# Performance work log

Hardware: AMD Instinct MI355X
Metric: run time of the kernel (lower is better)

## Reference

```python
import jax, jax.numpy as jnp
import numpy as np

D_MODEL = 768
D_INNER = 1536
D_STATE = 16
D_CONV = 4
DT_RANK = 48
N_LAYER = 4
VOCAB = 32000
B, L = 2, 1024


def rmsnorm(x, w, eps=1e-5):
    return x * jax.lax.rsqrt(jnp.mean(x * x, axis=-1, keepdims=True) + eps) * w


def depthwise_causal_conv(u, w):
    # u: (b, l, d_in), w: (d_in, k). torch pads both sides then truncates to l,
    # which equals left-pad by k-1 (causal).
    b, l, d = u.shape
    k = w.shape[1]
    up = jnp.pad(u, ((0, 0), (k - 1, 0), (0, 0)))
    out = jnp.zeros_like(u)
    for i in range(k):
        out = out + up[:, i:i + l, :] * w[:, i]
    return out


def selective_scan(u, delta, A, Bm, C, Dp):
    # u,delta: (b,l,d_in); A: (d_in,n); Bm,C: (b,l,n); Dp: (d_in,)
    dA = jnp.exp(delta[..., None] * A)                      # (b,l,d,n)
    dBu = delta[..., None] * Bm[:, :, None, :] * u[..., None]

    def step(h, inp):
        dA_t, dBu_t, C_t = inp
        h = dA_t * h + dBu_t                                 # (b,d,n)
        y = jnp.einsum('bdn,bn->bd', h, C_t)
        return h, y

    h0 = jnp.zeros_like(dA[:, 0])
    xs = (jnp.moveaxis(dA, 1, 0), jnp.moveaxis(dBu, 1, 0), jnp.moveaxis(C, 1, 0))
    _, ys = jax.lax.scan(step, h0, xs)                       # (l,b,d)
    return jnp.moveaxis(ys, 0, 1) + u * Dp


def setup_inputs() -> dict:
    key = jax.random.key(0)
    ks = jax.random.split(key, 16)
    s = lambda fan: 1.0 / np.sqrt(fan)
    inp = {}
    inp['text_input'] = jax.random.randint(ks[0], (B, L), 0, VOCAB)
    inp['visual_input'] = jax.random.normal(ks[1], (B, L, D_MODEL), dtype=jnp.float32)
    inp['embedding'] = jax.random.normal(ks[2], (VOCAB, D_MODEL), dtype=jnp.float32) * 0.02
    inp['norm_w'] = jnp.ones((N_LAYER, D_MODEL), dtype=jnp.float32)
    inp['norm_f_w'] = jnp.ones((D_MODEL,), dtype=jnp.float32)
    inp['in_proj_w'] = jax.random.normal(ks[3], (N_LAYER, 2 * D_INNER, D_MODEL)) * s(D_MODEL)
    inp['in_proj2_w'] = jax.random.normal(ks[4], (N_LAYER, D_INNER, D_MODEL)) * s(D_MODEL)
    inp['conv_w'] = jax.random.normal(ks[5], (N_LAYER, D_INNER, D_CONV)) * s(D_CONV)
    inp['conv_b'] = jax.random.normal(ks[6], (N_LAYER, D_INNER)) * 0.01
    inp['x_proj_w'] = jax.random.normal(ks[7], (N_LAYER, DT_RANK + D_STATE, D_INNER)) * s(D_INNER)
    inp['c_proj_w'] = jax.random.normal(ks[8], (N_LAYER, D_STATE, D_INNER)) * s(D_INNER)
    inp['dt_proj_w'] = jax.random.normal(ks[9], (N_LAYER, D_INNER, DT_RANK)) * s(DT_RANK)
    inp['dt_proj_b'] = jax.random.normal(ks[10], (N_LAYER, D_INNER)) * 0.01
    A = jnp.tile(jnp.arange(1, D_STATE + 1, dtype=jnp.float32)[None, :], (D_INNER, 1))
    inp['A_log'] = jnp.tile(jnp.log(A)[None], (N_LAYER, 1, 1))
    inp['D'] = jnp.ones((N_LAYER, D_INNER), dtype=jnp.float32)
    inp['out_proj_w'] = jax.random.normal(ks[11], (N_LAYER, D_MODEL, D_INNER)) * s(D_INNER)
    return inp


def reference(text_input, visual_input, embedding, norm_w, norm_f_w, in_proj_w,
              in_proj2_w, conv_w, conv_b, x_proj_w, c_proj_w, dt_proj_w,
              dt_proj_b, A_log, D, out_proj_w):
    x = embedding[text_input]  # (b,l,d_model)
    n_layer = A_log.shape[0]
    l = x.shape[1]
    for i in range(n_layer):
        q = rmsnorm(x, norm_w[i])
        v = rmsnorm(visual_input, norm_w[i])
        xr = q @ in_proj_w[i].T                               # (b,l,2*d_inner)
        vin = v @ in_proj2_w[i].T                             # (b,l,d_inner)
        t, res = jnp.split(xr, 2, axis=-1)
        t = depthwise_causal_conv(t, conv_w[i]) + conv_b[i]
        t = jax.nn.silu(t)
        # ssm
        A = -jnp.exp(A_log[i])
        x_dbl = t @ x_proj_w[i].T                             # (b,l,dt_rank+n)
        delta, Bm = jnp.split(x_dbl, [DT_RANK], axis=-1)
        C = vin @ c_proj_w[i].T                               # (b,l,n)
        delta = jax.nn.softplus(delta @ dt_proj_w[i].T + dt_proj_b[i])
        y = selective_scan(t, delta, A, Bm, C, D[i])
        y = y * jax.nn.silu(res)
        x = y @ out_proj_w[i].T + x
    x = rmsnorm(x, norm_f_w)
    return x @ embedding.T  # tied lm_head -> (b,l,vocab)
```

## Files before the change

kernel.cpp:

```cpp
#include <hip/hip_runtime.h>
#include <hip/hip_bf16.h>
#include <math.h>

#define B_ 2
#define L_ 1024
#define DM 768
#define DI 1536
#define DS 16
#define DR 48
#define NL 4
#define VOC 32000
#define BL (B_*L_)
#define NCH 32
#define LCH (L_/NCH)
#define KSPLIT 4

typedef __attribute__((ext_vector_type(8))) short short8;
typedef __attribute__((ext_vector_type(4))) float f32x4;

__device__ __forceinline__ float sigmoidf_(float x){ return 1.f/(1.f+expf(-x)); }
__device__ __forceinline__ float siluf_(float x){ return x*sigmoidf_(x); }
__device__ __forceinline__ float softplusf_(float x){ return fmaxf(x,0.f) + log1pf(expf(-fabsf(x))); }
__device__ __forceinline__ unsigned short f2bf(float f){
    unsigned u = __float_as_uint(f);
    u += 0x7FFFu + ((u >> 16) & 1u);
    return (unsigned short)(u >> 16);
}
__device__ __forceinline__ float bf2f(unsigned short h){
    return __uint_as_float((unsigned)h << 16);
}
__device__ __forceinline__ void gload_lds16(const unsigned short* g, unsigned short* l){
    __builtin_amdgcn_global_load_lds(
        (const __attribute__((address_space(1))) void*)g,
        (__attribute__((address_space(3))) void*)l, 16, 0, 0);
}

__global__ void cast_bf16_kernel(const float* __restrict__ in, unsigned short* __restrict__ out, int n4)
{
    for (int i = blockIdx.x*256 + threadIdx.x; i < n4; i += gridDim.x*256) {
        float4 v = ((const float4*)in)[i];
        ushort4 o;
        o.x = f2bf(v.x); o.y = f2bf(v.y); o.z = f2bf(v.z); o.w = f2bf(v.w);
        ((ushort4*)out)[i] = o;
    }
}

__global__ void cast_pair_kernel(const float* __restrict__ in,
                                 unsigned short* __restrict__ hi,
                                 unsigned short* __restrict__ lo, int n4)
{
    for (int i = blockIdx.x*256 + threadIdx.x; i < n4; i += gridDim.x*256) {
        float4 v = ((const float4*)in)[i];
        ushort4 h, l;
        h.x = f2bf(v.x); l.x = f2bf(v.x - bf2f(h.x));
        h.y = f2bf(v.y); l.y = f2bf(v.y - bf2f(h.y));
        h.z = f2bf(v.z); l.z = f2bf(v.z - bf2f(h.z));
        h.w = f2bf(v.w); l.w = f2bf(v.w - bf2f(h.w));
        ((ushort4*)hi)[i] = h;
        ((ushort4*)lo)[i] = l;
    }
}

__global__ void embed_kernel(const int* __restrict__ idx, const float* __restrict__ emb,
                             float* __restrict__ x)
{
    int i = blockIdx.x*256 + threadIdx.x;
    if (i >= BL*DM) return;
    int c = i % DM; int bl = i / DM;
    x[i] = emb[(size_t)idx[bl]*DM + c];
}

template<int MODE>
__global__ void rmsnorm_kernel(const float* __restrict__ in, const float* __restrict__ w,
                               void* __restrict__ outv, void* __restrict__ outv2)
{
    int row = blockIdx.x;
    const float* xr = in + (size_t)row*DM;
    float ss = 0.f;
    for (int c = threadIdx.x; c < DM; c += 256) { float v = xr[c]; ss += v*v; }
    #pragma unroll
    for (int o = 32; o > 0; o >>= 1) ss += __shfl_down(ss, o, 64);
    __shared__ float red[4];
    if ((threadIdx.x & 63) == 0) red[threadIdx.x >> 6] = ss;
    __syncthreads();
    float tot = red[0] + red[1] + red[2] + red[3];
    float scale = rsqrtf(tot * (1.f/DM) + 1e-5f);
    for (int c = threadIdx.x; c < DM; c += 256) {
        float v = xr[c]*scale*w[c];
        if (MODE == 0) ((float*)outv)[(size_t)row*DM + c] = v;
        else if (MODE == 1) ((unsigned short*)outv)[(size_t)row*DM + c] = f2bf(v);
        else {
            unsigned short h = f2bf(v);
            ((unsigned short*)outv)[(size_t)row*DM + c]  = h;
            ((unsigned short*)outv2)[(size_t)row*DM + c] = f2bf(v - bf2f(h));
        }
    }
}

template<int EPI>
__global__ __launch_bounds__(256) void gemm_mfma(
    const unsigned short* __restrict__ A, int lda,
    const unsigned short* __restrict__ W, int ldb,
    float* __restrict__ C, int ldc,
    const float* __restrict__ extra,
    int K)
{
    __shared__ unsigned short As[128*64];
    __shared__ unsigned short Bs[128*64];
    const int tid = threadIdx.x;
    const int bm = blockIdx.y*128, bn = blockIdx.x*128;
    const int l  = tid & 63;
    const int w  = tid >> 6;
    const int wr = (w >> 1)*64, wc = (w & 1)*64;
    const int lr = l & 15, lg = l >> 4;

    f32x4 zero4 = {0.f, 0.f, 0.f, 0.f};
    f32x4 acc[4][4];
    #pragma unroll
    for (int m = 0; m < 4; m++)
        #pragma unroll
        for (int n = 0; n < 4; n++) acc[m][n] = zero4;

    for (int k0 = 0; k0 < K; k0 += 64) {
        __syncthreads();
        #pragma unroll
        for (int i = 0; i < 4; i++) {
            int c   = i*256 + tid;
            int row = c >> 3;
            int kb  = c & 7;
            int kbs = (kb ^ (row & 7)) << 3;
            gload_lds16(A + (size_t)(bm+row)*lda + k0 + kbs, &As[c*8]);
            gload_lds16(W + (size_t)(bn+row)*ldb + k0 + kbs, &Bs[c*8]);
        }
        __syncthreads();
        #pragma unroll
        for (int kk = 0; kk < 2; kk++) {
            short8 af[4], bfr[4];
            #pragma unroll
            for (int m = 0; m < 4; m++) {
                int row = wr + m*16 + lr;
                int kb  = kk*4 + lg;
                af[m] = *(const short8*)&As[row*64 + ((kb ^ (row & 7)) << 3)];
            }
            #pragma unroll
            for (int n = 0; n < 4; n++) {
                int row = wc + n*16 + lr;
                int kb  = kk*4 + lg;
                bfr[n] = *(const short8*)&Bs[row*64 + ((kb ^ (row & 7)) << 3)];
            }
            #pragma unroll
            for (int m = 0; m < 4; m++)
                #pragma unroll
                for (int n = 0; n < 4; n++)
                    acc[m][n] = __builtin_amdgcn_mfma_f32_16x16x32_bf16(af[m], bfr[n], acc[m][n], 0, 0, 0);
        }
    }

    #pragma unroll
    for (int m = 0; m < 4; m++) {
        #pragma unroll
        for (int n = 0; n < 4; n++) {
            int col = bn + wc + n*16 + lr;
            #pragma unroll
            for (int r = 0; r < 4; r++) {
                int rowi = bm + wr + m*16 + lg*4 + r;
                float v = acc[m][n][r];
                if (EPI == 1) v += extra[(size_t)rowi*ldc + col];
                C[(size_t)rowi*ldc + col] = v;
            }
        }
    }
}

template<int EPI>
__global__ __launch_bounds__(256) void gemm_mfma2(
    const unsigned short* __restrict__ Ah, const unsigned short* __restrict__ Alo, int lda,
    const unsigned short* __restrict__ Wh, const unsigned short* __restrict__ Wlo, int ldb,
    float* __restrict__ C, int ldc,
    const float* __restrict__ extra,
    int K)
{
    __shared__ unsigned short Ash[128*64];
    __shared__ unsigned short Asl[128*64];
    __shared__ unsigned short Bsh[128*64];
    __shared__ unsigned short Bsl[128*64];
    const int tid = threadIdx.x;
    const int bm = blockIdx.y*128, bn = blockIdx.x*128;
    const int l  = tid & 63;
    const int w  = tid >> 6;
    const int wr = (w >> 1)*64, wc = (w & 1)*64;
    const int lr = l & 15, lg = l >> 4;

    f32x4 zero4 = {0.f, 0.f, 0.f, 0.f};
    f32x4 acc[4][4];
    #pragma unroll
    for (int m = 0; m < 4; m++)
        #pragma unroll
        for (int n = 0; n < 4; n++) acc[m][n] = zero4;

    for (int k0 = 0; k0 < K; k0 += 64) {
        __syncthreads();
        #pragma unroll
        for (int i = 0; i < 4; i++) {
            int c   = i*256 + tid;
            int row = c >> 3;
            int kb  = c & 7;
            int kbs = (kb ^ (row & 7)) << 3;
            const size_t ao = (size_t)(bm+row)*lda + k0 + kbs;
            const size_t bo = (size_t)(bn+row)*ldb + k0 + kbs;
            gload_lds16(Ah  + ao, &Ash[c*8]);
            gload_lds16(Alo + ao, &Asl[c*8]);
            gload_lds16(Wh  + bo, &Bsh[c*8]);
            gload_lds16(Wlo + bo, &Bsl[c*8]);
        }
        __syncthreads();
        #pragma unroll
        for (int kk = 0; kk < 2; kk++) {
            short8 ah[4], al[4], bh[4], bl[4];
            #pragma unroll
            for (int m = 0; m < 4; m++) {
                int row = wr + m*16 + lr;
                int so  = row*64 + (((kk*4 + lg) ^ (row & 7)) << 3);
                ah[m] = *(const short8*)&Ash[so];
                al[m] = *(const short8*)&Asl[so];
            }
            #pragma unroll
            for (int n = 0; n < 4; n++) {
                int row = wc + n*16 + lr;
                int so  = row*64 + (((kk*4 + lg) ^ (row & 7)) << 3);
                bh[n] = *(const short8*)&Bsh[so];
                bl[n] = *(const short8*)&Bsl[so];
            }
            #pragma unroll
            for (int m = 0; m < 4; m++)
                #pragma unroll
                for (int n = 0; n < 4; n++) {
                    acc[m][n] = __builtin_amdgcn_mfma_f32_16x16x32_bf16(al[m], bh[n], acc[m][n], 0, 0, 0);
                    acc[m][n] = __builtin_amdgcn_mfma_f32_16x16x32_bf16(ah[m], bl[n], acc[m][n], 0, 0, 0);
                    acc[m][n] = __builtin_amdgcn_mfma_f32_16x16x32_bf16(ah[m], bh[n], acc[m][n], 0, 0, 0);
                }
        }
    }

    #pragma unroll
    for (int m = 0; m < 4; m++) {
        #pragma unroll
        for (int n = 0; n < 4; n++) {
            int col = bn + wc + n*16 + lr;
            #pragma unroll
            for (int r = 0; r < 4; r++) {
                int rowi = bm + wr + m*16 + lg*4 + r;
                float v = acc[m][n][r];
                if (EPI == 1) v += extra[(size_t)rowi*ldc + col];
                C[(size_t)rowi*ldc + col] = v;
            }
        }
    }
}

template<int EPI>
__global__ __launch_bounds__(256) void gemm_tile(
    const float* __restrict__ A, int lda,
    const float* __restrict__ W, int ldb,
    float* __restrict__ C, int ldc,
    const float* __restrict__ extra,
    int K)
{
    __shared__ float As[8][128];
    __shared__ float Bs[8][128];
    const int bm = blockIdx.y * 128;
    const int bn = blockIdx.x * 128;
    const int tid = threadIdx.x;
    const int lr = tid >> 1;
    const int lh = (tid & 1) * 4;
    const int tr = tid >> 4;
    const int tc = tid & 15;

    float acc[8][8];
    #pragma unroll
    for (int i = 0; i < 8; i++)
        #pragma unroll
        for (int j = 0; j < 8; j++) acc[i][j] = 0.f;

    const float* Arow = A + (size_t)(bm + lr)*lda + lh;
    const float* Wrow = W + (size_t)(bn + lr)*ldb + lh;

    for (int k0 = 0; k0 < K; k0 += 8) {
        float4 av = *(const float4*)(Arow + k0);
        float4 wv = *(const float4*)(Wrow + k0);
        __syncthreads();
        As[lh+0][lr] = av.x; As[lh+1][lr] = av.y; As[lh+2][lr] = av.z; As[lh+3][lr] = av.w;
        Bs[lh+0][lr] = wv.x; Bs[lh+1][lr] = wv.y; Bs[lh+2][lr] = wv.z; Bs[lh+3][lr] = wv.w;
        __syncthreads();
        #pragma unroll
        for (int k = 0; k < 8; k++) {
            float a[8], b[8];
            *(float4*)(a)   = *(const float4*)&As[k][tr*8];
            *(float4*)(a+4) = *(const float4*)&As[k][tr*8+4];
            *(float4*)(b)   = *(const float4*)&Bs[k][tc*8];
            *(float4*)(b+4) = *(const float4*)&Bs[k][tc*8+4];
            #pragma unroll
            for (int i = 0; i < 8; i++)
                #pragma unroll
                for (int j = 0; j < 8; j++)
                    acc[i][j] = fmaf(a[i], b[j], acc[i][j]);
        }
    }

    #pragma unroll
    for (int i = 0; i < 8; i++) {
        int row = bm + tr*8 + i;
        float* crow = C + (size_t)row*ldc + bn + tc*8;
        float v[8];
        if (EPI == 2) {
            const float* bia = extra + bn + tc*8;
            #pragma unroll
            for (int j = 0; j < 8; j++) v[j] = softplusf_(acc[i][j] + bia[j]);
        } else {
            #pragma unroll
            for (int j = 0; j < 8; j++) v[j] = acc[i][j];
        }
        *(float4*)(crow)   = make_float4(v[0],v[1],v[2],v[3]);
        *(float4*)(crow+4) = make_float4(v[4],v[5],v[6],v[7]);
    }
}

__global__ __launch_bounds__(256) void gemm_skinny(
    const float* __restrict__ A, int lda,
    const float* __restrict__ W, int ldb,
    float* __restrict__ partial,
    int M, int N, int K)
{
    int klen = K / gridDim.z;
    int kbeg = blockIdx.z * klen;
    __shared__ float As[64][33];
    __shared__ float Ws[16][33];
    int tid = threadIdx.x;
    int bm = blockIdx.y*64, bn = blockIdx.x*16;
    int ar = tid >> 2, ak = (tid & 3)*8;
    int wr = tid >> 4, wk = (tid & 15)*2;
    int tr = tid >> 4, tc = tid & 15;

    float acc[4] = {0.f,0.f,0.f,0.f};
    for (int k0 = kbeg; k0 < kbeg + klen; k0 += 32) {
        float4 a0 = *(const float4*)(A + (size_t)(bm+ar)*lda + k0 + ak);
        float4 a1 = *(const float4*)(A + (size_t)(bm+ar)*lda + k0 + ak + 4);
        float2 wv = *(const float2*)(W + (size_t)(bn+wr)*ldb + k0 + wk);
        __syncthreads();
        As[ar][ak+0]=a0.x; As[ar][ak+1]=a0.y; As[ar][ak+2]=a0.z; As[ar][ak+3]=a0.w;
        As[ar][ak+4]=a1.x; As[ar][ak+5]=a1.y; As[ar][ak+6]=a1.z; As[ar][ak+7]=a1.w;
        Ws[wr][wk] = wv.x; Ws[wr][wk+1] = wv.y;
        __syncthreads();
        #pragma unroll 8
        for (int k = 0; k < 32; k++) {
            float b = Ws[tc][k];
            #pragma unroll
            for (int i = 0; i < 4; i++) acc[i] = fmaf(As[tr*4+i][k], b, acc[i]);
        }
    }
    #pragma unroll
    for (int i = 0; i < 4; i++)
        partial[((size_t)blockIdx.z*M + bm + tr*4 + i)*N + bn + tc] = acc[i];
}

__global__ void reduce_splitk(const float* __restrict__ partial, float* __restrict__ out, int MN)
{
    int i = blockIdx.x*256 + threadIdx.x;
    if (i >= MN) return;
    float s = 0.f;
    #pragma unroll
    for (int z = 0; z < KSPLIT; z++) s += partial[(size_t)z*MN + i];
    out[i] = s;
}

__global__ void conv_silu_kernel(const float* __restrict__ xr, const float* __restrict__ cw,
                                 const float* __restrict__ cb, float* __restrict__ t)
{
    int i = blockIdx.x*256 + threadIdx.x;
    if (i >= BL*DI) return;
    int d = i % DI; int bl = i / DI; int l = bl % L_; int b = bl / L_;
    const float* base = xr + (size_t)b*L_*(2*DI);
    float acc = cb[d];
    #pragma unroll
    for (int q = 0; q < 4; q++) {
        int ll = l - 3 + q;
        if (ll >= 0) acc = fmaf(base[(size_t)ll*(2*DI) + d], cw[d*4+q], acc);
    }
    t[i] = siluf_(acc);
}

__global__ void scan_p1(const float* __restrict__ delta, const float* __restrict__ t,
                        const float* __restrict__ xdbl, const float* __restrict__ A_log,
                        float* __restrict__ Aprod, float* __restrict__ Bacc)
{
    int idx = blockIdx.x*256 + threadIdx.x;
    if (idx >= B_*NCH*DI) return;
    int d = idx % DI; int c = (idx/DI) % NCH; int b = idx/(DI*NCH);
    float Ad[16];
    #pragma unroll
    for (int n = 0; n < 16; n++) Ad[n] = -expf(A_log[d*16+n]);
    float P[16], S[16];
    #pragma unroll
    for (int n = 0; n < 16; n++) { P[n] = 1.f; S[n] = 0.f; }
    for (int s = 0; s < LCH; s++) {
        int bl = b*L_ + c*LCH + s;
        float dt = delta[(size_t)bl*DI + d];
        float u  = t[(size_t)bl*DI + d];
        const float* Bp = xdbl + (size_t)bl*64 + 48;
        #pragma unroll
        for (int n = 0; n < 16; n++) {
            float a  = expf(dt*Ad[n]);
            float bu = dt*Bp[n]*u;
            P[n] *= a;
            S[n] = fmaf(a, S[n], bu);
        }
    }
    size_t o = (size_t)idx*16;
    #pragma unroll
    for (int n = 0; n < 16; n++) { Aprod[o+n] = P[n]; Bacc[o+n] = S[n]; }
}

__global__ void scan_p2(const float* __restrict__ Aprod, const float* __restrict__ Bacc,
                        float* __restrict__ Hinit)
{
    int idx = blockIdx.x*256 + threadIdx.x;
    if (idx >= B_*DI) return;
    int d = idx % DI, b = idx / DI;
    float h[16];
    #pragma unroll
    for (int n = 0; n < 16; n++) h[n] = 0.f;
    for (int c = 0; c < NCH; c++) {
        size_t o = (((size_t)b*NCH + c)*DI + d)*16;
        #pragma unroll
        for (int n = 0; n < 16; n++) Hinit[o+n] = h[n];
        #pragma unroll
        for (int n = 0; n < 16; n++) h[n] = fmaf(Aprod[o+n], h[n], Bacc[o+n]);
    }
}

__global__ void scan_p3(const float* __restrict__ delta, const float* __restrict__ t,
                        const float* __restrict__ xdbl, const float* __restrict__ Cb,
                        const float* __restrict__ A_log, const float* __restrict__ Dp,
                        const float* __restrict__ Hinit, const float* __restrict__ xr,
                        unsigned short* __restrict__ zh, unsigned short* __restrict__ zl)
{
    int idx = blockIdx.x*256 + threadIdx.x;
    if (idx >= B_*NCH*DI) return;
    int d = idx % DI; int c = (idx/DI) % NCH; int b = idx/(DI*NCH);
    float Ad[16];
    #pragma unroll
    for (int n = 0; n < 16; n++) Ad[n] = -expf(A_log[d*16+n]);
    float h[16];
    size_t ho = (size_t)idx*16;
    #pragma unroll
    for (int n = 0; n < 16; n++) h[n] = Hinit[ho+n];
    float Dd = Dp[d];
    for (int s = 0; s < LCH; s++) {
        int bl = b*L_ + c*LCH + s;
        float dt = delta[(size_t)bl*DI + d];
        float u  = t[(size_t)bl*DI + d];
        const float* Bp = xdbl + (size_t)bl*64 + 48;
        const float* Cp = Cb + (size_t)bl*16;
        float y = 0.f;
        #pragma unroll
        for (int n = 0; n < 16; n++) {
            float a = expf(dt*Ad[n]);
            h[n] = fmaf(a, h[n], dt*Bp[n]*u);
            y = fmaf(h[n], Cp[n], y);
        }
        y = fmaf(u, Dd, y);
        float r = xr[(size_t)bl*(2*DI) + DI + d];
        float zv = y * siluf_(r);
        unsigned short hh = f2bf(zv);
        zh[(size_t)bl*DI + d] = hh;
        zl[(size_t)bl*DI + d] = f2bf(zv - bf2f(hh));
    }
}

extern "C" void kernel_launch(void* const* d_in, const int* in_sizes, int n_in,
                              void* d_out, int out_size, void* d_ws, size_t ws_size,
                              hipStream_t stream)
{
    const int*   text     = (const int*)  d_in[0];
    const float* visual   = (const float*)d_in[1];
    const float* emb      = (const float*)d_in[2];
    const float* norm_w   = (const float*)d_in[3];
    const float* norm_f_w = (const float*)d_in[4];
    const float* in_proj  = (const float*)d_in[5];
    const float* in_proj2 = (const float*)d_in[6];
    const float* conv_w   = (const float*)d_in[7];
    const float* conv_b   = (const float*)d_in[8];
    const float* x_proj   = (const float*)d_in[9];
    const float* c_proj   = (const float*)d_in[10];
    const float* dt_w     = (const float*)d_in[11];
    const float* dt_b     = (const float*)d_in[12];
    const float* A_log    = (const float*)d_in[13];
    const float* Dp       = (const float*)d_in[14];
    const float* out_proj = (const float*)d_in[15];
    float* out = (float*)d_out;

    float* ws = (float*)d_ws;
    size_t off = 0;
    float* x     = ws + off; off += (size_t)BL*DM;
    float* xr    = ws + off; off += (size_t)BL*2*DI;
    float* vin   = ws + off; off += (size_t)BL*DI;
    float* tb    = ws + off; off += (size_t)BL*DI;
    float* dl    = ws + off; off += (size_t)BL*DI;
    float* xdbl  = ws + off; off += (size_t)BL*64;
    float* Cb    = ws + off; off += (size_t)BL*16;
    float* Aprod = ws + off; off += (size_t)B_*NCH*DI*DS;
    float* Bacc  = ws + off; off += (size_t)B_*NCH*DI*DS;
    float* Hinit = ws + off; off += (size_t)B_*NCH*DI*DS;
    float* part  = ws + off; off += (size_t)KSPLIT*BL*64;

    unsigned short* bfb = (unsigned short*)(ws + off);
    size_t bo = 0;
    unsigned short* emb_bf = bfb + bo; bo += (size_t)VOC*DM;
    unsigned short* wA_h   = bfb + bo; bo += (size_t)2*DI*DM;
    unsigned short* wA_l   = bfb + bo; bo += (size_t)2*DI*DM;
    unsigned short* wB_h   = bfb + bo; bo += (size_t)DI*DM;
    unsigned short* wB_l   = bfb + bo; bo += (size_t)DI*DM;
    unsigned short* wO_h   = bfb + bo; bo += (size_t)DM*DI;
    unsigned short* wO_l   = bfb + bo; bo += (size_t)DM*DI;
    unsigned short* q_h    = bfb + bo; bo += (size_t)BL*DM;
    unsigned short* q_l    = bfb + bo; bo += (size_t)BL*DM;
    unsigned short* v_h    = bfb + bo; bo += (size_t)BL*DM;
    unsigned short* v_l    = bfb + bo; bo += (size_t)BL*DM;
    unsigned short* z_h    = bfb + bo; bo += (size_t)BL*DI;
    unsigned short* z_l    = bfb + bo; bo += (size_t)BL*DI;
    unsigned short* xn_bf  = bfb + bo; bo += (size_t)BL*DM;

    dim3 blk(256);
    dim3 cgrid(2048);

    cast_bf16_kernel<<<cgrid, blk, 0, stream>>>(emb, emb_bf, VOC*DM/4);

    embed_kernel<<<dim3((BL*DM)/256), blk, 0, stream>>>(text, emb, x);

    for (int i = 0; i < NL; i++) {
        const float* nw = norm_w + (size_t)i*DM;
        rmsnorm_kernel<2><<<dim3(BL), blk, 0, stream>>>(x, nw, q_h, q_l);
        rmsnorm_kernel<2><<<dim3(BL), blk, 0, stream>>>(visual, nw, v_h, v_l);

        cast_pair_kernel<<<cgrid, blk, 0, stream>>>(in_proj  + (size_t)i*2*DI*DM, wA_h, wA_l, 2*DI*DM/4);
        cast_pair_kernel<<<cgrid, blk, 0, stream>>>(in_proj2 + (size_t)i*DI*DM,   wB_h, wB_l, DI*DM/4);
        cast_pair_kernel<<<cgrid, blk, 0, stream>>>(out_proj + (size_t)i*DM*DI,   wO_h, wO_l, DM*DI/4);

        gemm_mfma2<0><<<dim3(2*DI/128, BL/128), blk, 0, stream>>>(
            q_h, q_l, DM, wA_h, wA_l, DM, xr, 2*DI, nullptr, DM);
        gemm_mfma2<0><<<dim3(DI/128, BL/128), blk, 0, stream>>>(
            v_h, v_l, DM, wB_h, wB_l, DM, vin, DI, nullptr, DM);

        conv_silu_kernel<<<dim3((BL*DI)/256), blk, 0, stream>>>(
            xr, conv_w + (size_t)i*DI*4, conv_b + (size_t)i*DI, tb);

        gemm_skinny<<<dim3(64/16, BL/64, KSPLIT), blk, 0, stream>>>(
            tb, DI, x_proj + (size_t)i*(DR+DS)*DI, DI, part, BL, 64, DI);
        reduce_splitk<<<dim3((BL*64)/256), blk, 0, stream>>>(part, xdbl, BL*64);

        gemm_skinny<<<dim3(1, BL/64, KSPLIT), blk, 0, stream>>>(
            vin, DI, c_proj + (size_t)i*DS*DI, DI, part, BL, 16, DI);
        reduce_splitk<<<dim3((BL*16)/256), blk, 0, stream>>>(part, Cb, BL*16);

        gemm_tile<2><<<dim3(DI/128, BL/128), blk, 0, stream>>>(
            xdbl, 64, dt_w + (size_t)i*DI*DR, DR, dl, DI, dt_b + (size_t)i*DI, DR);

        const float* Al = A_log + (size_t)i*DI*DS;
        scan_p1<<<dim3((B_*NCH*DI)/256), blk, 0, stream>>>(dl, tb, xdbl, Al, Aprod, Bacc);
        scan_p2<<<dim3((B_*DI+255)/256), blk, 0, stream>>>(Aprod, Bacc, Hinit);
        scan_p3<<<dim3((B_*NCH*DI)/256), blk, 0, stream>>>(dl, tb, xdbl, Cb, Al,
            Dp + (size_t)i*DI, Hinit, xr, z_h, z_l);

        gemm_mfma2<1><<<dim3(DM/128, BL/128), blk, 0, stream>>>(
            z_h, z_l, DI, wO_h, wO_l, DI, x, DM, x, DI);
    }

    rmsnorm_kernel<1><<<dim3(BL), blk, 0, stream>>>(x, norm_f_w, xn_bf, nullptr);
    gemm_mfma<0><<<dim3(VOC/128, BL/128), blk, 0, stream>>>(
        xn_bf, DM, emb_bf, DM, out, VOC, nullptr, DM);
}
```

Before: 1.952 ms.

## Fuse paired launches, merge x_proj/c_proj GEMMs, remap and stream LM head

Several pairs of kernels become single launches: the two rmsnorms, the three weight casts, the two in-projection GEMMs, and the x_proj/c_proj skinny GEMMs with their split-K reductions, which now write one 80-wide buffer. The scan kernels read B and C as float4 from that buffer, and the skinny GEMM uses vectorized LDS reads. The LM head GEMM swaps its grid to iterate M fastest, adds an XCD-aware block remap, and writes logits with nontemporal stores. The aim is less launch overhead, fewer passes over memory and better L2 reuse of embedding tiles, at the cost of branchy combined kernels and padded LDS rows.

```diff
diff --git a/kernel.cpp b/kernel.cpp
--- a/kernel.cpp
+++ b/kernel.cpp
@@ -14,6 +14,7 @@
 #define NCH 32
 #define LCH (L_/NCH)
 #define KSPLIT 4
+#define NXD 80
 
 typedef __attribute__((ext_vector_type(8))) short short8;
 typedef __attribute__((ext_vector_type(4))) float f32x4;
@@ -45,19 +46,25 @@
     }
 }
 
-__global__ void cast_pair_kernel(const float* __restrict__ in,
-                                 unsigned short* __restrict__ hi,
-                                 unsigned short* __restrict__ lo, int n4)
-{
-    for (int i = blockIdx.x*256 + threadIdx.x; i < n4; i += gridDim.x*256) {
-        float4 v = ((const float4*)in)[i];
-        ushort4 h, l;
-        h.x = f2bf(v.x); l.x = f2bf(v.x - bf2f(h.x));
-        h.y = f2bf(v.y); l.y = f2bf(v.y - bf2f(h.y));
-        h.z = f2bf(v.z); l.z = f2bf(v.z - bf2f(h.z));
-        h.w = f2bf(v.w); l.w = f2bf(v.w - bf2f(h.w));
-        ((ushort4*)hi)[i] = h;
-        ((ushort4*)lo)[i] = l;
+__global__ void cast_pair3_kernel(
+    const float* __restrict__ s1, unsigned short* __restrict__ h1, unsigned short* __restrict__ l1, int n1,
+    const float* __restrict__ s2, unsigned short* __restrict__ h2, unsigned short* __restrict__ l2, int n2,
+    const float* __restrict__ s3, unsigned short* __restrict__ h3, unsigned short* __restrict__ l3, int n3)
+{
+    int total = n1 + n2 + n3;
+    for (int i = blockIdx.x*256 + threadIdx.x; i < total; i += gridDim.x*256) {
+        const float* s; unsigned short *h, *l; int j;
+        if (i < n1)           { s = s1; h = h1; l = l1; j = i; }
+        else if (i < n1 + n2) { s = s2; h = h2; l = l2; j = i - n1; }
+        else                  { s = s3; h = h3; l = l3; j = i - n1 - n2; }
+        float4 v = ((const float4*)s)[j];
+        ushort4 hh, ll;
+        hh.x = f2bf(v.x); ll.x = f2bf(v.x - bf2f(hh.x));
+        hh.y = f2bf(v.y); ll.y = f2bf(v.y - bf2f(hh.y));
+        hh.z = f2bf(v.z); ll.z = f2bf(v.z - bf2f(hh.z));
+        hh.w = f2bf(v.w); ll.w = f2bf(v.w - bf2f(hh.w));
+        ((ushort4*)h)[j] = hh;
+        ((ushort4*)l)[j] = ll;
     }
 }
 
@@ -70,12 +77,35 @@
     x[i] = emb[(size_t)idx[bl]*DM + c];
 }
 
-template<int MODE>
-__global__ void rmsnorm_kernel(const float* __restrict__ in, const float* __restrict__ w,
-                               void* __restrict__ outv, void* __restrict__ outv2)
+__global__ void rmsnorm_bf_kernel(const float* __restrict__ in, const float* __restrict__ w,
+                                  unsigned short* __restrict__ out)
 {
     int row = blockIdx.x;
     const float* xr = in + (size_t)row*DM;
+    float ss = 0.f;
+    for (int c = threadIdx.x; c < DM; c += 256) { float v = xr[c]; ss += v*v; }
+    #pragma unroll
+    for (int o = 32; o > 0; o >>= 1) ss += __shfl_down(ss, o, 64);
+    __shared__ float red[4];
+    if ((threadIdx.x & 63) == 0) red[threadIdx.x >> 6] = ss;
+    __syncthreads();
+    float tot = red[0] + red[1] + red[2] + red[3];
+    float scale = rsqrtf(tot * (1.f/DM) + 1e-5f);
+    for (int c = threadIdx.x; c < DM; c += 256)
+        out[(size_t)row*DM + c] = f2bf(xr[c]*scale*w[c]);
+}
+
+__global__ void rmsnorm_dual_kernel(const float* __restrict__ x, const float* __restrict__ vis,
+                                    const float* __restrict__ w,
+                                    unsigned short* __restrict__ qh, unsigned short* __restrict__ ql,
+                                    unsigned short* __restrict__ vh, unsigned short* __restrict__ vl)
+{
+    int row = blockIdx.x;
+    bool first = row < BL;
+    int r = first ? row : row - BL;
+    const float* xr = (first ? x : vis) + (size_t)r*DM;
+    unsigned short* oh = (first ? qh : vh) + (size_t)r*DM;
+    unsigned short* ol = (first ? ql : vl) + (size_t)r*DM;
     float ss = 0.f;
     for (int c = threadIdx.x; c < DM; c += 256) { float v = xr[c]; ss += v*v; }
     #pragma unroll
@@ -87,28 +117,30 @@
     float scale = rsqrtf(tot * (1.f/DM) + 1e-5f);
     for (int c = threadIdx.x; c < DM; c += 256) {
         float v = xr[c]*scale*w[c];
-        if (MODE == 0) ((float*)outv)[(size_t)row*DM + c] = v;
-        else if (MODE == 1) ((unsigned short*)outv)[(size_t)row*DM + c] = f2bf(v);
-        else {
-            unsigned short h = f2bf(v);
-            ((unsigned short*)outv)[(size_t)row*DM + c]  = h;
-            ((unsigned short*)outv2)[(size_t)row*DM + c] = f2bf(v - bf2f(h));
-        }
-    }
-}
-
-template<int EPI>
-__global__ __launch_bounds__(256) void gemm_mfma(
+        unsigned short h = f2bf(v);
+        oh[c] = h;
+        ol[c] = f2bf(v - bf2f(h));
+    }
+}
+
+__global__ __launch_bounds__(256) void gemm_head(
     const unsigned short* __restrict__ A, int lda,
     const unsigned short* __restrict__ W, int ldb,
-    float* __restrict__ C, int ldc,
-    const float* __restrict__ extra,
-    int K)
+    float* __restrict__ C, int ldc, int K)
 {
     __shared__ unsigned short As[128*64];
     __shared__ unsigned short Bs[128*64];
     const int tid = threadIdx.x;
-    const int bm = blockIdx.y*128, bn = blockIdx.x*128;
+
+    int nwg  = gridDim.x*gridDim.y;
+    int flat = blockIdx.y*gridDim.x + blockIdx.x;
+    if ((nwg & 7) == 0) {
+        int q = nwg >> 3;
+        flat = (flat & 7)*q + (flat >> 3);
+    }
+    const int bm = (flat % gridDim.x)*128;
+    const int bn = (flat / gridDim.x)*128;
+
     const int l  = tid & 63;
     const int w  = tid >> 6;
     const int wr = (w >> 1)*64, wc = (w & 1)*64;
@@ -139,14 +171,12 @@
             #pragma unroll
             for (int m = 0; m < 4; m++) {
                 int row = wr + m*16 + lr;
-                int kb  = kk*4 + lg;
-                af[m] = *(const short8*)&As[row*64 + ((kb ^ (row & 7)) << 3)];
+                af[m] = *(const short8*)&As[row*64 + (((kk*4+lg) ^ (row & 7)) << 3)];
             }
             #pragma unroll
             for (int n = 0; n < 4; n++) {
                 int row = wc + n*16 + lr;
-                int kb  = kk*4 + lg;
-                bfr[n] = *(const short8*)&Bs[row*64 + ((kb ^ (row & 7)) << 3)];
+                bfr[n] = *(const short8*)&Bs[row*64 + (((kk*4+lg) ^ (row & 7)) << 3)];
             }
             #pragma unroll
             for (int m = 0; m < 4; m++)
@@ -157,35 +187,27 @@
     }
 
     #pragma unroll
-    for (int m = 0; m < 4; m++) {
+    for (int m = 0; m < 4; m++)
         #pragma unroll
         for (int n = 0; n < 4; n++) {
             int col = bn + wc + n*16 + lr;
             #pragma unroll
             for (int r = 0; r < 4; r++) {
                 int rowi = bm + wr + m*16 + lg*4 + r;
-                float v = acc[m][n][r];
-                if (EPI == 1) v += extra[(size_t)rowi*ldc + col];
-                C[(size_t)rowi*ldc + col] = v;
+                __builtin_nontemporal_store(acc[m][n][r], &C[(size_t)rowi*ldc + col]);
             }
         }
-    }
 }
 
 template<int EPI>
-__global__ __launch_bounds__(256) void gemm_mfma2(
+__device__ __forceinline__ void mfma2_body(
     const unsigned short* __restrict__ Ah, const unsigned short* __restrict__ Alo, int lda,
     const unsigned short* __restrict__ Wh, const unsigned short* __restrict__ Wlo, int ldb,
-    float* __restrict__ C, int ldc,
-    const float* __restrict__ extra,
-    int K)
-{
-    __shared__ unsigned short Ash[128*64];
-    __shared__ unsigned short Asl[128*64];
-    __shared__ unsigned short Bsh[128*64];
-    __shared__ unsigned short Bsl[128*64];
+    float* __restrict__ C, int ldc, const float* __restrict__ extra,
+    int K, int bm, int bn,
+    unsigned short* Ash, unsigned short* Asl, unsigned short* Bsh, unsigned short* Bsl)
+{
     const int tid = threadIdx.x;
-    const int bm = blockIdx.y*128, bn = blockIdx.x*128;
     const int l  = tid & 63;
     const int w  = tid >> 6;
     const int wr = (w >> 1)*64, wc = (w & 1)*64;
@@ -243,7 +265,7 @@
     }
 
     #pragma unroll
-    for (int m = 0; m < 4; m++) {
+    for (int m = 0; m < 4; m++)
         #pragma unroll
         for (int n = 0; n < 4; n++) {
             int col = bn + wc + n*16 + lr;
@@ -255,7 +277,42 @@
                 C[(size_t)rowi*ldc + col] = v;
             }
         }
-    }
+}
+
+template<int EPI>
+__global__ __launch_bounds__(256) void gemm_mfma2(
+    const unsigned short* __restrict__ Ah, const unsigned short* __restrict__ Alo, int lda,
+    const unsigned short* __restrict__ Wh, const unsigned short* __restrict__ Wlo, int ldb,
+    float* __restrict__ C, int ldc, const float* __restrict__ extra, int K)
+{
+    __shared__ unsigned short Ash[128*64];
+    __shared__ unsigned short Asl[128*64];
+    __shared__ unsigned short Bsh[128*64];
+    __shared__ unsigned short Bsl[128*64];
+    mfma2_body<EPI>(Ah, Alo, lda, Wh, Wlo, ldb, C, ldc, extra, K,
+                    blockIdx.y*128, blockIdx.x*128, Ash, Asl, Bsh, Bsl);
+}
+
+__global__ __launch_bounds__(256) void gemm_mfma2_dual(
+    const unsigned short* __restrict__ Ah1, const unsigned short* __restrict__ Al1,
+    const unsigned short* __restrict__ Wh1, const unsigned short* __restrict__ Wl1,
+    float* __restrict__ C1, int ldc1, int nb1,
+    const unsigned short* __restrict__ Ah2, const unsigned short* __restrict__ Al2,
+    const unsigned short* __restrict__ Wh2, const unsigned short* __restrict__ Wl2,
+    float* __restrict__ C2, int ldc2,
+    int lda, int ldb, int K)
+{
+    __shared__ unsigned short Ash[128*64];
+    __shared__ unsigned short Asl[128*64];
+    __shared__ unsigned short Bsh[128*64];
+    __shared__ unsigned short Bsl[128*64];
+    int bx = blockIdx.x;
+    if (bx < nb1)
+        mfma2_body<0>(Ah1, Al1, lda, Wh1, Wl1, ldb, C1, ldc1, nullptr, K,
+                      blockIdx.y*128, bx*128, Ash, Asl, Bsh, Bsl);
+    else
+        mfma2_body<0>(Ah2, Al2, lda, Wh2, Wl2, ldb, C2, ldc2, nullptr, K,
+                      blockIdx.y*128, (bx-nb1)*128, Ash, Asl, Bsh, Bsl);
 }
 
 template<int EPI>
@@ -325,18 +382,23 @@
     }
 }
 
-__global__ __launch_bounds__(256) void gemm_skinny(
-    const float* __restrict__ A, int lda,
-    const float* __restrict__ W, int ldb,
-    float* __restrict__ partial,
-    int M, int N, int K)
+__global__ __launch_bounds__(256) void gemm_skinny2(
+    const float* __restrict__ A1, const float* __restrict__ A2, int lda,
+    const float* __restrict__ W1, const float* __restrict__ W2, int ldb,
+    float* __restrict__ partial, int K)
 {
     int klen = K / gridDim.z;
     int kbeg = blockIdx.z * klen;
-    __shared__ float As[64][33];
-    __shared__ float Ws[16][33];
+    __shared__ float As[64][36];
+    __shared__ float Ws[16][36];
     int tid = threadIdx.x;
-    int bm = blockIdx.y*64, bn = blockIdx.x*16;
+    int bx = blockIdx.x;
+    bool isC = (bx == 4);
+    const float* A = isC ? A2 : A1;
+    const float* W = isC ? W2 : W1;
+    int bn = isC ? 0 : bx*16;
+    int colbase = isC ? 64 : bx*16;
+    int bm = blockIdx.y*64;
     int ar = tid >> 2, ak = (tid & 3)*8;
     int wr = tid >> 4, wk = (tid & 15)*2;
     int tr = tid >> 4, tc = tid & 15;
@@ -347,20 +409,26 @@
         float4 a1 = *(const float4*)(A + (size_t)(bm+ar)*lda + k0 + ak + 4);
         float2 wv = *(const float2*)(W + (size_t)(bn+wr)*ldb + k0 + wk);
         __syncthreads();
-        As[ar][ak+0]=a0.x; As[ar][ak+1]=a0.y; As[ar][ak+2]=a0.z; As[ar][ak+3]=a0.w;
-        As[ar][ak+4]=a1.x; As[ar][ak+5]=a1.y; As[ar][ak+6]=a1.z; As[ar][ak+7]=a1.w;
+        *(float4*)&As[ar][ak]   = a0;
+        *(float4*)&As[ar][ak+4] = a1;
         Ws[wr][wk] = wv.x; Ws[wr][wk+1] = wv.y;
         __syncthreads();
-        #pragma unroll 8
-        for (int k = 0; k < 32; k++) {
-            float b = Ws[tc][k];
-            #pragma unroll
-            for (int i = 0; i < 4; i++) acc[i] = fmaf(As[tr*4+i][k], b, acc[i]);
+        #pragma unroll
+        for (int k = 0; k < 32; k += 4) {
+            float4 wv4 = *(const float4*)&Ws[tc][k];
+            #pragma unroll
+            for (int i = 0; i < 4; i++) {
+                float4 av4 = *(const float4*)&As[tr*4+i][k];
+                acc[i] = fmaf(av4.x, wv4.x, acc[i]);
+                acc[i] = fmaf(av4.y, wv4.y, acc[i]);
+                acc[i] = fmaf(av4.z, wv4.z, acc[i]);
+                acc[i] = fmaf(av4.w, wv4.w, acc[i]);
+            }
         }
     }
     #pragma unroll
     for (int i = 0; i < 4; i++)
-        partial[((size_t)blockIdx.z*M + bm + tr*4 + i)*N + bn + tc] = acc[i];
+        partial[((size_t)blockIdx.z*BL + bm + tr*4 + i)*NXD + colbase + tc] = acc[i];
 }
 
 __global__ void reduce_splitk(const float* __restrict__ partial, float* __restrict__ out, int MN)
@@ -406,13 +474,19 @@
         int bl = b*L_ + c*LCH + s;
         float dt = delta[(size_t)bl*DI + d];
         float u  = t[(size_t)bl*DI + d];
-        const float* Bp = xdbl + (size_t)bl*64 + 48;
+        const float4* Bp4 = (const float4*)(xdbl + (size_t)bl*NXD + 48);
+        float Bv[16];
+        #pragma unroll
+        for (int q = 0; q < 4; q++) {
+            float4 bv = Bp4[q];
+            Bv[q*4+0]=bv.x; Bv[q*4+1]=bv.y; Bv[q*4+2]=bv.z; Bv[q*4+3]=bv.w;
+        }
+        float du = dt*u;
         #pragma unroll
         for (int n = 0; n < 16; n++) {
             float a  = expf(dt*Ad[n]);
-            float bu = dt*Bp[n]*u;
             P[n] *= a;
-            S[n] = fmaf(a, S[n], bu);
+            S[n] = fmaf(a, S[n], du*Bv[n]);
         }
     }
     size_t o = (size_t)idx*16;
@@ -439,7 +513,7 @@
 }
 
 __global__ void scan_p3(const float* __restrict__ delta, const float* __restrict__ t,
-                        const float* __restrict__ xdbl, const float* __restrict__ Cb,
+                        const float* __restrict__ xdbl,
                         const float* __restrict__ A_log, const float* __restrict__ Dp,
                         const float* __restrict__ Hinit, const float* __restrict__ xr,
                         unsigned short* __restrict__ zh, unsigned short* __restrict__ zl)
@@ -459,14 +533,22 @@
         int bl = b*L_ + c*LCH + s;
         float dt = delta[(size_t)bl*DI + d];
         float u  = t[(size_t)bl*DI + d];
-        const float* Bp = xdbl + (size_t)bl*64 + 48;
-        const float* Cp = Cb + (size_t)bl*16;
+        const float4* Bp4 = (const float4*)(xdbl + (size_t)bl*NXD + 48);
+        const float4* Cp4 = (const float4*)(xdbl + (size_t)bl*NXD + 64);
+        float Bv[16], Cv[16];
+        #pragma unroll
+        for (int q = 0; q < 4; q++) {
+            float4 bv = Bp4[q]; float4 cv = Cp4[q];
+            Bv[q*4+0]=bv.x; Bv[q*4+1]=bv.y; Bv[q*4+2]=bv.z; Bv[q*4+3]=bv.w;
+            Cv[q*4+0]=cv.x; Cv[q*4+1]=cv.y; Cv[q*4+2]=cv.z; Cv[q*4+3]=cv.w;
+        }
+        float du = dt*u;
         float y = 0.f;
         #pragma unroll
         for (int n = 0; n < 16; n++) {
             float a = expf(dt*Ad[n]);
-            h[n] = fmaf(a, h[n], dt*Bp[n]*u);
-            y = fmaf(h[n], Cp[n], y);
+            h[n] = fmaf(a, h[n], du*Bv[n]);
+            y = fmaf(h[n], Cv[n], y);
         }
         y = fmaf(u, Dd, y);
         float r = xr[(size_t)bl*(2*DI) + DI + d];
@@ -506,12 +588,11 @@
     float* vin   = ws + off; off += (size_t)BL*DI;
     float* tb    = ws + off; off += (size_t)BL*DI;
     float* dl    = ws + off; off += (size_t)BL*DI;
-    float* xdbl  = ws + off; off += (size_t)BL*64;
-    float* Cb    = ws + off; off += (size_t)BL*16;
+    float* xdbl  = ws + off; off += (size_t)BL*NXD;
     float* Aprod = ws + off; off += (size_t)B_*NCH*DI*DS;
     float* Bacc  = ws + off; off += (size_t)B_*NCH*DI*DS;
     float* Hinit = ws + off; off += (size_t)B_*NCH*DI*DS;
-    float* part  = ws + off; off += (size_t)KSPLIT*BL*64;
+    float* part  = ws + off; off += (size_t)KSPLIT*BL*NXD;
 
     unsigned short* bfb = (unsigned short*)(ws + off);
     size_t bo = 0;
@@ -539,43 +620,42 @@
 
     for (int i = 0; i < NL; i++) {
         const float* nw = norm_w + (size_t)i*DM;
-        rmsnorm_kernel<2><<<dim3(BL), blk, 0, stream>>>(x, nw, q_h, q_l);
-        rmsnorm_kernel<2><<<dim3(BL), blk, 0, stream>>>(visual, nw, v_h, v_l);
-
-        cast_pair_kernel<<<cgrid, blk, 0, stream>>>(in_proj  + (size_t)i*2*DI*DM, wA_h, wA_l, 2*DI*DM/4);
-        cast_pair_kernel<<<cgrid, blk, 0, stream>>>(in_proj2 + (size_t)i*DI*DM,   wB_h, wB_l, DI*DM/4);
-        cast_pair_kernel<<<cgrid, blk, 0, stream>>>(out_proj + (size_t)i*DM*DI,   wO_h, wO_l, DM*DI/4);
-
-        gemm_mfma2<0><<<dim3(2*DI/128, BL/128), blk, 0, stream>>>(
-            q_h, q_l, DM, wA_h, wA_l, DM, xr, 2*DI, nullptr, DM);
-        gemm_mfma2<0><<<dim3(DI/128, BL/128), blk, 0, stream>>>(
-            v_h, v_l, DM, wB_h, wB_l, DM, vin, DI, nullptr, DM);
+
+        rmsnorm_dual_kernel<<<dim3(2*BL), blk, 0, stream>>>(
+            x, visual, nw, q_h, q_l, v_h, v_l);
+
+        cast_pair3_kernel<<<cgrid, blk, 0, stream>>>(
+            in_proj  + (size_t)i*2*DI*DM, wA_h, wA_l, 2*DI*DM/4,
+            in_proj2 + (size_t)i*DI*DM,   wB_h, wB_l, DI*DM/4,
+            out_proj + (size_t)i*DM*DI,   wO_h, wO_l, DM*DI/4);
+
+        gemm_mfma2_dual<<<dim3(2*DI/128 + DI/128, BL/128), blk, 0, stream>>>(
+            q_h, q_l, wA_h, wA_l, xr, 2*DI, 2*DI/128,
+            v_h, v_l, wB_h, wB_l, vin, DI,
+            DM, DM, DM);
 
         conv_silu_kernel<<<dim3((BL*DI)/256), blk, 0, stream>>>(
             xr, conv_w + (size_t)i*DI*4, conv_b + (size_t)i*DI, tb);
 
-        gemm_skinny<<<dim3(64/16, BL/64, KSPLIT), blk, 0, stream>>>(
-            tb, DI, x_proj + (size_t)i*(DR+DS)*DI, DI, part, BL, 64, DI);
-        reduce_splitk<<<dim3((BL*64)/256), blk, 0, stream>>>(part, xdbl, BL*64);
-
-        gemm_skinny<<<dim3(1, BL/64, KSPLIT), blk, 0, stream>>>(
-            vin, DI, c_proj + (size_t)i*DS*DI, DI, part, BL, 16, DI);
-        reduce_splitk<<<dim3((BL*16)/256), blk, 0, stream>>>(part, Cb, BL*16);
+        gemm_skinny2<<<dim3(5, BL/64, KSPLIT), blk, 0, stream>>>(
+            tb, vin, DI, x_proj + (size_t)i*(DR+DS)*DI, c_proj + (size_t)i*DS*DI, DI,
+            part, DI);
+        reduce_splitk<<<dim3((BL*NXD)/256), blk, 0, stream>>>(part, xdbl, BL*NXD);
 
         gemm_tile<2><<<dim3(DI/128, BL/128), blk, 0, stream>>>(
-            xdbl, 64, dt_w + (size_t)i*DI*DR, DR, dl, DI, dt_b + (size_t)i*DI, DR);
+            xdbl, NXD, dt_w + (size_t)i*DI*DR, DR, dl, DI, dt_b + (size_t)i*DI, DR);
 
         const float* Al = A_log + (size_t)i*DI*DS;
         scan_p1<<<dim3((B_*NCH*DI)/256), blk, 0, stream>>>(dl, tb, xdbl, Al, Aprod, Bacc);
         scan_p2<<<dim3((B_*DI+255)/256), blk, 0, stream>>>(Aprod, Bacc, Hinit);
-        scan_p3<<<dim3((B_*NCH*DI)/256), blk, 0, stream>>>(dl, tb, xdbl, Cb, Al,
+        scan_p3<<<dim3((B_*NCH*DI)/256), blk, 0, stream>>>(dl, tb, xdbl, Al,
             Dp + (size_t)i*DI, Hinit, xr, z_h, z_l);
 
         gemm_mfma2<1><<<dim3(DM/128, BL/128), blk, 0, stream>>>(
             z_h, z_l, DI, wO_h, wO_l, DI, x, DM, x, DI);
     }
 
-    rmsnorm_kernel<1><<<dim3(BL), blk, 0, stream>>>(x, norm_f_w, xn_bf, nullptr);
-    gemm_mfma<0><<<dim3(VOC/128, BL/128), blk, 0, stream>>>(
-        xn_bf, DM, emb_bf, DM, out, VOC, nullptr, DM);
-}
+    rmsnorm_bf_kernel<<<dim3(BL), blk, 0, stream>>>(x, norm_f_w, xn_bf);
+    gemm_head<<<dim3(BL/128, VOC/128), blk, 0, stream>>>(
+        xn_bf, DM, emb_bf, DM, out, VOC, DM);
+}
```

New measurement: 1.721 ms. 1.13x faster.
